# Kernel tuning notes

Measured on AMD Instinct MI355X. Metric: run time of the kernel, lower is better.

Reference implementation:

```python
import jax, jax.numpy as jnp
import numpy as np

DIM, NH, HD = 1536, 12, 128
C = HD // 2            # 64 complex (half) dims per head
BANDS = (C - 2 * (C // 3), C // 3, C // 3)   # (22, 21, 21) for T/H/W
EPS = 1e-6
F, Hg, Wg = 6, 20, 32
S = F * Hg * Wg
MAX_LEN = 1024


def _rope_tables(max_len=MAX_LEN):
    # Wan-style 1D rope params per band, concatenated along channel dim -> [max_len, 64]
    pos = np.arange(max_len, dtype=np.float64)
    cos_l, sin_l = [], []
    for bd in BANDS:
        inv = 1.0 / (10000.0 ** (np.arange(bd, dtype=np.float64) / bd))
        ang = np.outer(pos, inv)
        cos_l.append(np.cos(ang))
        sin_l.append(np.sin(ang))
    return (np.concatenate(cos_l, 1).astype(np.float32),
            np.concatenate(sin_l, 1).astype(np.float32))


def setup_inputs() -> dict:
    key = jax.random.key(0)
    ks = jax.random.split(key, 8)
    std = 0.02
    fc, fs = _rope_tables()
    return {
        "x": jax.random.normal(ks[0], (1, S, DIM), jnp.float32),
        "Wq": jax.random.normal(ks[1], (DIM, DIM), jnp.float32) * std,
        "bq": jnp.zeros((DIM,), jnp.float32),
        "Wk": jax.random.normal(ks[2], (DIM, DIM), jnp.float32) * std,
        "bk": jnp.zeros((DIM,), jnp.float32),
        "Wv": jax.random.normal(ks[3], (DIM, DIM), jnp.float32) * std,
        "bv": jnp.zeros((DIM,), jnp.float32),
        "Wo": jax.random.normal(ks[4], (DIM, DIM), jnp.float32) * std,
        "bo": jnp.zeros((DIM,), jnp.float32),
        "gq": jnp.ones((DIM,), jnp.float32),
        "gk": jnp.ones((DIM,), jnp.float32),
        "freqs_cos": jnp.asarray(fc),
        "freqs_sin": jnp.asarray(fs),
        "f": F, "h": Hg, "w": Wg,
    }


def _rmsnorm(t, g):
    t = t.astype(jnp.float32)
    return t * jax.lax.rsqrt(jnp.mean(t * t, axis=-1, keepdims=True) + EPS) * g


def _grid_freqs(tab, f, h, w):
    # tab: [max_len, 64] -> [f*h*w, 64] via T/H/W band broadcast (mirrors torch expand+cat)
    o1, o2 = BANDS[0], BANDS[0] + BANDS[1]
    t = jnp.broadcast_to(tab[:f, None, None, :o1], (f, h, w, BANDS[0]))
    hh = jnp.broadcast_to(tab[None, :h, None, o1:o2], (f, h, w, BANDS[1]))
    ww = jnp.broadcast_to(tab[None, None, :w, o2:C], (f, h, w, BANDS[2]))
    return jnp.concatenate([t, hh, ww], axis=-1).reshape(f * h * w, 1, C)


def _rope_apply(t, fc, fs):
    # t: [B, S, n, d]; complex mul (a+ib)*(cos+isin) on pairs of channels
    B, Sl, n, d = t.shape
    tr = t.astype(jnp.float32).reshape(B, Sl, n, C, 2)
    a, b = tr[..., 0], tr[..., 1]
    fc = fc[None]  # [1, S, 1, C]
    fs = fs[None]
    out_r = a * fc - b * fs
    out_i = a * fs + b * fc
    return jnp.stack([out_r, out_i], axis=-1).reshape(B, Sl, n, d)


def reference(x, Wq, bq, Wk, bk, Wv, bv, Wo, bo, gq, gk, freqs_cos, freqs_sin, f, h, w):
    B, Sl, _ = x.shape
    q = _rmsnorm(x @ Wq.T + bq, gq).reshape(B, Sl, NH, HD)
    k = _rmsnorm(x @ Wk.T + bk, gk).reshape(B, Sl, NH, HD)
    v = (x @ Wv.T + bv).reshape(B, Sl, NH, HD)

    fc = _grid_freqs(freqs_cos, f, h, w)
    fs = _grid_freqs(freqs_sin, f, h, w)
    q = _rope_apply(q, fc, fs)
    k = _rope_apply(k, fc, fs)

    scale = 1.0 / jnp.sqrt(jnp.float32(HD))
    scores = jnp.einsum('bqnd,bknd->bnqk', q, k) * scale
    p = jax.nn.softmax(scores, axis=-1)
    o = jnp.einsum('bnqk,bknd->bqnd', p, v.astype(jnp.float32))
    o = o.reshape(B, Sl, DIM)
    return o @ Wo.T + bo
```

## Files before the change

kernel.cpp:

```cpp
#include <hip/hip_runtime.h>
#include <hip/hip_bf16.h>
#include <cstdint>

#define DIM 1536
#define NHEADS 12
#define HD 128
#define SEQ 3840
#define SCL2F 0.1275365308119098f
#define THRRAW 90.50966799187809f

typedef float f32x4 __attribute__((ext_vector_type(4)));
typedef __bf16 bf16x8 __attribute__((ext_vector_type(8)));
typedef __bf16 bf16x4 __attribute__((ext_vector_type(4)));
typedef __bf16 bf16x2 __attribute__((ext_vector_type(2)));
typedef unsigned int u32;
typedef u32 u32x4 __attribute__((ext_vector_type(4)));

#define GLLD(g, l) __builtin_amdgcn_global_load_lds( \
    (const __attribute__((address_space(1))) void*)(g), \
    (__attribute__((address_space(3))) void*)(l), 16, 0, 0)

__global__ __launch_bounds__(256) void cvt_bf16_5(
    const float* __restrict__ s0, const float* __restrict__ s1, const float* __restrict__ s2,
    const float* __restrict__ s3, const float* __restrict__ s4,
    __bf16* __restrict__ d0, __bf16* __restrict__ d1, __bf16* __restrict__ d2,
    __bf16* __restrict__ d3, __bf16* __restrict__ d4,
    int n4_0, int n4_w) {
    const float* src; __bf16* dst; int n4;
    switch (blockIdx.y) {
        case 0: src = s0; dst = d0; n4 = n4_0; break;
        case 1: src = s1; dst = d1; n4 = n4_w; break;
        case 2: src = s2; dst = d2; n4 = n4_w; break;
        case 3: src = s3; dst = d3; n4 = n4_w; break;
        default: src = s4; dst = d4; n4 = n4_w; break;
    }
    int i = blockIdx.x * 256 + threadIdx.x;
    if (i < n4) {
        f32x4 v = ((const f32x4*)src)[i];
        bf16x4 o;
        o[0] = (__bf16)v[0]; o[1] = (__bf16)v[1];
        o[2] = (__bf16)v[2]; o[3] = (__bf16)v[3];
        ((bf16x4*)dst)[i] = o;
    }
}

template <int OUTF32>
__global__ __launch_bounds__(256, 2) void gemm256(
    const __bf16* __restrict__ A,
    const __bf16* __restrict__ B0, const __bf16* __restrict__ B1, const __bf16* __restrict__ B2,
    const float* __restrict__ bias0, const float* __restrict__ bias1, const float* __restrict__ bias2,
    void* __restrict__ C0v, void* __restrict__ C1v, void* __restrict__ C2v,
    int N, int K) {
    const __bf16* B = B0; const float* bias = bias0; void* Cv = C0v;
    if (blockIdx.z == 1) { B = B1; bias = bias1; Cv = C1v; }
    else if (blockIdx.z == 2) { B = B2; bias = bias2; Cv = C2v; }

    __shared__ __bf16 sA[3][256 * 32];
    __shared__ __bf16 sB[3][128 * 32];

    const int t = threadIdx.x;
    const int wid = t >> 6, lane = t & 63;
    const int lr = lane & 15, lg = lane >> 4;
    const int wr = (wid >> 1) * 128, wc = (wid & 1) * 64;

    const __bf16* pa = A + ((long long)blockIdx.y * 256 + (t >> 2)) * K + (t & 3) * 8;
    const __bf16* pb = B + ((long long)blockIdx.x * 128 + (t >> 2)) * K + (t & 3) * 8;
    const int ldsbase = wid * 512;

    auto stage = [&](int kk, int bufi) {
#pragma unroll
        for (int r = 0; r < 4; r++)
            GLLD(pa + (long long)(r * 64) * K + kk, &sA[bufi][r * 2048 + ldsbase]);
#pragma unroll
        for (int r = 0; r < 2; r++)
            GLLD(pb + (long long)(r * 64) * K + kk, &sB[bufi][r * 2048 + ldsbase]);
    };

    f32x4 acc[8][4] = {};
    const int NT = K / 32;

    stage(0, 0);
    stage(32, 1);
    asm volatile("s_waitcnt vmcnt(6)" ::: "memory");
    __builtin_amdgcn_s_barrier();
    __builtin_amdgcn_sched_barrier(0);

    int c0 = 0, c2 = 2;
#pragma unroll 1
    for (int i = 0; i < NT; i++) {
        const __bf16* sAc = &sA[0][0] + c0 * (256 * 32);
        const __bf16* sBc = &sB[0][0] + c0 * (128 * 32);
        bf16x8 af[8], bfr[4];
#pragma unroll
        for (int mI = 0; mI < 8; mI++)
            af[mI] = *(const bf16x8*)(sAc + (wr + mI * 16 + lr) * 32 + lg * 8);
#pragma unroll
        for (int nI = 0; nI < 4; nI++)
            bfr[nI] = *(const bf16x8*)(sBc + (wc + nI * 16 + lr) * 32 + lg * 8);
        if (i + 2 < NT) stage((i + 2) * 32, c2);

        __builtin_amdgcn_s_setprio(1);
#pragma unroll
        for (int mI = 0; mI < 8; mI++) {
            acc[mI][0] = __builtin_amdgcn_mfma_f32_16x16x32_bf16(af[mI], bfr[0], acc[mI][0], 0, 0, 0);
            acc[mI][1] = __builtin_amdgcn_mfma_f32_16x16x32_bf16(af[mI], bfr[1], acc[mI][1], 0, 0, 0);
        }
        __builtin_amdgcn_s_setprio(0);
        __builtin_amdgcn_s_barrier();
        __builtin_amdgcn_s_setprio(1);
#pragma unroll
        for (int mI = 0; mI < 8; mI++) {
            acc[mI][2] = __builtin_amdgcn_mfma_f32_16x16x32_bf16(af[mI], bfr[2], acc[mI][2], 0, 0, 0);
            acc[mI][3] = __builtin_amdgcn_mfma_f32_16x16x32_bf16(af[mI], bfr[3], acc[mI][3], 0, 0, 0);
        }
        __builtin_amdgcn_s_setprio(0);

        if (i + 2 < NT) asm volatile("s_waitcnt vmcnt(6)" ::: "memory");
        else            asm volatile("s_waitcnt vmcnt(0)" ::: "memory");
        __builtin_amdgcn_s_barrier();
        __builtin_amdgcn_sched_barrier(0);
        c0 = (c0 == 2) ? 0 : c0 + 1;
        c2 = (c2 == 2) ? 0 : c2 + 1;
    }

    const int cb = blockIdx.x * 128 + wc;
    const int rb_ = blockIdx.y * 256 + wr;
#pragma unroll
    for (int nI = 0; nI < 4; nI++) {
        int col = cb + nI * 16 + lr;
        float bv = bias[col];
#pragma unroll
        for (int mI = 0; mI < 8; mI++) {
            int row0 = rb_ + mI * 16 + lg * 4;
#pragma unroll
            for (int r = 0; r < 4; r++) {
                float v = acc[mI][nI][r] + bv;
                if (OUTF32) ((float*)Cv)[(long long)(row0 + r) * N + col] = v;
                else ((__bf16*)Cv)[(long long)(row0 + r) * N + col] = (__bf16)v;
            }
        }
    }
}

__global__ __launch_bounds__(256) void norm_rope2(
    const __bf16* __restrict__ qpre, const __bf16* __restrict__ kpre,
    const float* __restrict__ gq, const float* __restrict__ gk,
    const float* __restrict__ fcos, const float* __restrict__ fsin,
    __bf16* __restrict__ Qb, __bf16* __restrict__ Kb) {
    const __bf16* pre = blockIdx.y ? kpre : qpre;
    const float* gvec = blockIdx.y ? gk : gq;
    __bf16* out = blockIdx.y ? Kb : Qb;
    const int s = blockIdx.x;
    const int t = threadIdx.x;
    float a[3], b[3];
    float ss = 0.f;
#pragma unroll
    for (int j = 0; j < 3; j++) {
        int p = t + 256 * j;
        bf16x2 v = *(const bf16x2*)(pre + (size_t)s * DIM + 2 * p);
        a[j] = (float)v[0]; b[j] = (float)v[1];
        ss += a[j] * a[j] + b[j] * b[j];
    }
    for (int off = 32; off; off >>= 1) ss += __shfl_down(ss, off);
    __shared__ float red[4];
    if ((t & 63) == 0) red[t >> 6] = ss;
    __syncthreads();
    float mean = (red[0] + red[1] + red[2] + red[3]) * (1.f / DIM);
    float rms = rsqrtf(mean + 1e-6f);
    const int fi = s / 640, hi2 = (s % 640) >> 5, wi = s & 31;
#pragma unroll
    for (int j = 0; j < 3; j++) {
        int p = t + 256 * j;
        int c = p & 63;
        int pos = (c < 22) ? fi : ((c < 43) ? hi2 : wi);
        float fc = fcos[pos * 64 + c];
        float fs = fsin[pos * 64 + c];
        float av = a[j] * rms * gvec[2 * p];
        float bv = b[j] * rms * gvec[2 * p + 1];
        float orr = av * fc - bv * fs;
        float oi = av * fs + bv * fc;
        int hh = p >> 6;
        bf16x2 o; o[0] = (__bf16)orr; o[1] = (__bf16)oi;
        *(bf16x2*)(out + ((size_t)hh * SEQ + s) * HD + 2 * c) = o;
    }
}

__global__ __launch_bounds__(256) void transpose_bf16(
    const __bf16* __restrict__ in, __bf16* __restrict__ out) {
    __shared__ __bf16 tile[64][68];
    const int t = threadIdx.x;
    const int sb = blockIdx.x * 64, cb = blockIdx.y * 64;
    const int tx = t & 15, ty = t >> 4;
#pragma unroll
    for (int i = 0; i < 4; i++) {
        int r = ty + i * 16;
        bf16x4 v = *(const bf16x4*)(in + (size_t)(sb + r) * DIM + cb + tx * 4);
        *(bf16x4*)&tile[r][tx * 4] = v;
    }
    __syncthreads();
    int s0 = sb + tx * 4;
    int j = (s0 >> 2) & 7;
    int u = (j < 4) ? (j << 1) : ((j << 1) - 7);
    int sp = (s0 & ~31) + (u << 2);
#pragma unroll
    for (int i = 0; i < 4; i++) {
        int c = ty + i * 16;
        bf16x4 v;
        v[0] = tile[tx * 4 + 0][c]; v[1] = tile[tx * 4 + 1][c];
        v[2] = tile[tx * 4 + 2][c]; v[3] = tile[tx * 4 + 3][c];
        *(bf16x4*)(out + (size_t)(cb + c) * SEQ + sp) = v;
    }
}

__global__ __launch_bounds__(384, 1) void attn(
    const __bf16* __restrict__ Q, const __bf16* __restrict__ Kk,
    const __bf16* __restrict__ Vp, __bf16* __restrict__ O) {
    __shared__ __bf16 Ks[2][64 * 128];
    __shared__ __bf16 Vs[2][128 * 64];
    const int bid = blockIdx.x;
    const int task = (bid & 7) * 30 + (bid >> 3);
    const int h = task / 20;
    const int qb = task % 20;
    const int t = threadIdx.x;
    const int wv = t >> 6;
    const int lane = t & 63;
    const int lq = lane & 15, g = lane >> 4;
    const int q0 = qb * 192 + wv * 32;
    const __bf16* Qh = Q + (size_t)h * SEQ * HD;
    const __bf16* Kh = Kk + (size_t)h * SEQ * HD;
    const __bf16* Vh = Vp + (size_t)h * HD * SEQ;
    bf16x8 qf[2][4];
#pragma unroll
    for (int qg = 0; qg < 2; qg++)
#pragma unroll
        for (int c = 0; c < 4; c++)
            qf[qg][c] = *(const bf16x8*)(Qh + (size_t)(q0 + qg * 16 + lq) * HD + c * 32 + g * 8);
    f32x4 acc[8][2] = {};
    float m[2] = {-1e30f, -1e30f};
    float lp[2] = {0.f, 0.f};
    const int krow_in = lane >> 4;
    const int vrow_in = lane >> 3;
    const int vce = (((lane & 7) ^ (lane >> 3))) * 8;
    auto stage = [&](int kv0, int b) {
        for (int c = wv; c < 32; c += 6) {
            if (c < 16) {
                int r = c * 4 + krow_in;
                int cb = ((lane & 15) * 16) ^ ((r & 7) << 4);
                GLLD(Kh + (size_t)(kv0 + r) * HD + (cb >> 1), &Ks[b][c * 512]);
            } else {
                int cc = c - 16;
                int rd = cc * 8 + vrow_in;
                GLLD(Vh + (size_t)rd * SEQ + kv0 + vce, &Vs[b][cc * 512]);
            }
        }
    };
    stage(0, 0);
    int buf = 0;
    const int kswz = (lq & 7) << 3;
#pragma unroll 1
    for (int i = 0; i < 60; i++) {
        __syncthreads();
        if (i + 1 < 60) stage((i + 1) * 64, buf ^ 1);
        const __bf16* Kb_ = &Ks[buf][0];
        const __bf16* Vb_ = &Vs[buf][0];
#pragma unroll
        for (int s = 0; s < 2; s++) {
            f32x4 sc[2][2] = {};
            __builtin_amdgcn_s_setprio(1);
#pragma unroll
            for (int c = 0; c < 4; c++) {
                int cb = (c * 32 + g * 8) ^ kswz;
                bf16x8 k0 = *(const bf16x8*)(Kb_ + (s * 32 + lq) * 128 + cb);
                bf16x8 k1 = *(const bf16x8*)(Kb_ + (s * 32 + 16 + lq) * 128 + cb);
                sc[0][0] = __builtin_amdgcn_mfma_f32_16x16x32_bf16(k0, qf[0][c], sc[0][0], 0, 0, 0);
                sc[0][1] = __builtin_amdgcn_mfma_f32_16x16x32_bf16(k0, qf[1][c], sc[0][1], 0, 0, 0);
                sc[1][0] = __builtin_amdgcn_mfma_f32_16x16x32_bf16(k1, qf[0][c], sc[1][0], 0, 0, 0);
                sc[1][1] = __builtin_amdgcn_mfma_f32_16x16x32_bf16(k1, qf[1][c], sc[1][1], 0, 0, 0);
            }
            __builtin_amdgcn_s_setprio(0);

            bf16x8 vf[8];
#pragma unroll
            for (int dt = 0; dt < 8; dt++)
                vf[dt] = *(const bf16x8*)(Vb_ + (dt * 16 + lq) * 64 + ((s * 32 + g * 8) ^ kswz));

            bf16x8 pa[2];
#pragma unroll
            for (int qg = 0; qg < 2; qg++) {
                float pm = fmaxf(fmaxf(fmaxf(sc[0][qg][0], sc[0][qg][1]), fmaxf(sc[0][qg][2], sc[0][qg][3])),
                                 fmaxf(fmaxf(sc[1][qg][0], sc[1][qg][1]), fmaxf(sc[1][qg][2], sc[1][qg][3])));
                if (!__all(pm <= m[qg] + THRRAW)) {
                    pm = fmaxf(pm, __shfl_xor(pm, 16));
                    pm = fmaxf(pm, __shfl_xor(pm, 32));
                    float mn = fmaxf(m[qg], pm);
                    float al = __builtin_amdgcn_exp2f(SCL2F * (m[qg] - mn));
                    m[qg] = mn; lp[qg] *= al;
#pragma unroll
                    for (int dt = 0; dt < 8; dt++)
#pragma unroll
                        for (int r = 0; r < 4; r++) acc[dt][qg][r] *= al;
                }
                float ms = SCL2F * m[qg];
                float p[8], ls = 0.f;
#pragma unroll
                for (int r = 0; r < 4; r++) { p[r] = __builtin_amdgcn_exp2f(SCL2F * sc[0][qg][r] - ms); ls += p[r]; }
#pragma unroll
                for (int r = 0; r < 4; r++) { p[4 + r] = __builtin_amdgcn_exp2f(SCL2F * sc[1][qg][r] - ms); ls += p[4 + r]; }
                lp[qg] += ls;
#pragma unroll
                for (int i2 = 0; i2 < 8; i2++) pa[qg][i2] = (__bf16)p[i2];
            }
            __builtin_amdgcn_s_setprio(1);
#pragma unroll
            for (int dt = 0; dt < 8; dt++) {
                acc[dt][0] = __builtin_amdgcn_mfma_f32_16x16x32_bf16(vf[dt], pa[0], acc[dt][0], 0, 0, 0);
                acc[dt][1] = __builtin_amdgcn_mfma_f32_16x16x32_bf16(vf[dt], pa[1], acc[dt][1], 0, 0, 0);
            }
            __builtin_amdgcn_s_setprio(0);
        }
        buf ^= 1;
    }
#pragma unroll
    for (int qg = 0; qg < 2; qg++) {
        float lps = lp[qg];
        lps += __shfl_xor(lps, 16);
        lps += __shfl_xor(lps, 32);
        float inv = 1.f / lps;
#pragma unroll
        for (int dt = 0; dt < 8; dt++) {
            bf16x4 o;
#pragma unroll
            for (int r = 0; r < 4; r++) o[r] = (__bf16)(acc[dt][qg][r] * inv);
            *(bf16x4*)(O + (size_t)(q0 + qg * 16 + lq) * DIM + h * HD + dt * 16 + g * 4) = o;
        }
    }
}

extern "C" void kernel_launch(void* const* d_in, const int* in_sizes, int n_in,
                              void* d_out, int out_size, void* d_ws, size_t ws_size,
                              hipStream_t stream) {
    const float* x = (const float*)d_in[0];
    const float* Wq = (const float*)d_in[1];
    const float* bq = (const float*)d_in[2];
    const float* Wk = (const float*)d_in[3];
    const float* bk = (const float*)d_in[4];
    const float* Wv = (const float*)d_in[5];
    const float* bv = (const float*)d_in[6];
    const float* Wo = (const float*)d_in[7];
    const float* bo = (const float*)d_in[8];
    const float* gq = (const float*)d_in[9];
    const float* gk = (const float*)d_in[10];
    const float* fcos = (const float*)d_in[11];
    const float* fsin = (const float*)d_in[12];
    float* out = (float*)d_out;

    char* p = (char*)d_ws;
    const size_t SZ_SD = (size_t)SEQ * DIM * 2;
    const size_t SZ_W = (size_t)DIM * DIM * 2;
    __bf16* xb   = (__bf16*)p;  p += SZ_SD;
    __bf16* Wqb  = (__bf16*)p;  p += SZ_W;
    __bf16* Wkb  = (__bf16*)p;  p += SZ_W;
    __bf16* Wvb  = (__bf16*)p;  p += SZ_W;
    __bf16* Wob  = (__bf16*)p;  p += SZ_W;
    __bf16* qpre = (__bf16*)p;  p += SZ_SD;
    __bf16* kpre = (__bf16*)p;  p += SZ_SD;
    __bf16* vpre = (__bf16*)p;  p += SZ_SD;
    __bf16* Kb   = (__bf16*)p;  p += SZ_SD;
    __bf16* Vtb  = (__bf16*)p;  p += SZ_SD;
    __bf16* Qb = xb;
    __bf16* ob = qpre;

    const int n4_x = SEQ * DIM / 4;
    const int n4_w = DIM * DIM / 4;
    cvt_bf16_5<<<dim3((n4_x + 255) / 256, 5), 256, 0, stream>>>(
        x, Wq, Wk, Wv, Wo, xb, Wqb, Wkb, Wvb, Wob, n4_x, n4_w);

    gemm256<0><<<dim3(DIM / 128, SEQ / 256, 3), 256, 0, stream>>>(
        xb, Wqb, Wkb, Wvb, bq, bk, bv, qpre, kpre, vpre, DIM, DIM);

    norm_rope2<<<dim3(SEQ, 2), 256, 0, stream>>>(qpre, kpre, gq, gk, fcos, fsin, Qb, Kb);
    transpose_bf16<<<dim3(SEQ / 64, DIM / 64), 256, 0, stream>>>(vpre, Vtb);

    attn<<<dim3(240), 384, 0, stream>>>(Qb, Kb, Vtb, ob);

    gemm256<1><<<dim3(DIM / 128, SEQ / 256, 1), 256, 0, stream>>>(
        ob, Wob, Wob, Wob, bo, bo, bo, out, out, out, DIM, DIM);
}
```

Before: 287.1 us.

## Split attention into smaller 64-query blocks with 32-key tiles for higher occupancy

The attention kernel moves from 240 blocks of 6 waves, each wave covering 32 queries over 64-key tiles, to 720 blocks of 4 waves, each wave covering 16 queries over 32-key tiles, with launch bounds allowing 4 blocks per CU. The aim is to fill all CUs more evenly and put more waves on each CU so that latency and the serial softmax section are better hidden. In exchange, each K/V tile held in LDS is reused by fewer queries, K/V are fetched from global memory three times as often, there are twice as many barrier iterations, and the new V LDS layout drops the XOR swizzle, which may cause bank conflicts.

After: 284.9 us. Within noise of the previous version (-0.8%).

```diff
diff --git a/kernel.cpp b/kernel.cpp
--- a/kernel.cpp
+++ b/kernel.cpp
@@ -212,127 +212,120 @@
     }
 }
 
-__global__ __launch_bounds__(384, 1) void attn(
+__global__ __launch_bounds__(256, 4) void attn(
     const __bf16* __restrict__ Q, const __bf16* __restrict__ Kk,
     const __bf16* __restrict__ Vp, __bf16* __restrict__ O) {
-    __shared__ __bf16 Ks[2][64 * 128];
-    __shared__ __bf16 Vs[2][128 * 64];
+    __shared__ __bf16 Ks[2][32 * 128];
+    __shared__ __bf16 Vs[2][128 * 32];
     const int bid = blockIdx.x;
-    const int task = (bid & 7) * 30 + (bid >> 3);
-    const int h = task / 20;
-    const int qb = task % 20;
+    const int task = (bid & 7) * 90 + (bid >> 3);
+    const int h = task / 60;
+    const int qb = task % 60;
     const int t = threadIdx.x;
     const int wv = t >> 6;
     const int lane = t & 63;
     const int lq = lane & 15, g = lane >> 4;
-    const int q0 = qb * 192 + wv * 32;
+    const int q0 = qb * 64 + wv * 16;
     const __bf16* Qh = Q + (size_t)h * SEQ * HD;
     const __bf16* Kh = Kk + (size_t)h * SEQ * HD;
     const __bf16* Vh = Vp + (size_t)h * HD * SEQ;
-    bf16x8 qf[2][4];
-#pragma unroll
-    for (int qg = 0; qg < 2; qg++)
-#pragma unroll
-        for (int c = 0; c < 4; c++)
-            qf[qg][c] = *(const bf16x8*)(Qh + (size_t)(q0 + qg * 16 + lq) * HD + c * 32 + g * 8);
-    f32x4 acc[8][2] = {};
-    float m[2] = {-1e30f, -1e30f};
-    float lp[2] = {0.f, 0.f};
+
+    bf16x8 qf[4];
+#pragma unroll
+    for (int c = 0; c < 4; c++)
+        qf[c] = *(const bf16x8*)(Qh + (size_t)(q0 + lq) * HD + c * 32 + g * 8);
+
+    f32x4 acc[8] = {};
+    float m = -1e30f;
+    float lp = 0.f;
+
     const int krow_in = lane >> 4;
-    const int vrow_in = lane >> 3;
-    const int vce = (((lane & 7) ^ (lane >> 3))) * 8;
+    const int vrow_in = lane >> 2;
+    const int vce = (lane & 3) * 8;
     auto stage = [&](int kv0, int b) {
-        for (int c = wv; c < 32; c += 6) {
-            if (c < 16) {
+#pragma unroll
+        for (int c = wv; c < 16; c += 4) {
+            if (c < 8) {
                 int r = c * 4 + krow_in;
                 int cb = ((lane & 15) * 16) ^ ((r & 7) << 4);
                 GLLD(Kh + (size_t)(kv0 + r) * HD + (cb >> 1), &Ks[b][c * 512]);
             } else {
-                int cc = c - 16;
-                int rd = cc * 8 + vrow_in;
+                int cc = c - 8;
+                int rd = cc * 16 + vrow_in;
                 GLLD(Vh + (size_t)rd * SEQ + kv0 + vce, &Vs[b][cc * 512]);
             }
         }
     };
+
     stage(0, 0);
     int buf = 0;
     const int kswz = (lq & 7) << 3;
 #pragma unroll 1
-    for (int i = 0; i < 60; i++) {
+    for (int i = 0; i < 120; i++) {
         __syncthreads();
-        if (i + 1 < 60) stage((i + 1) * 64, buf ^ 1);
+        if (i + 1 < 120) stage((i + 1) * 32, buf ^ 1);
         const __bf16* Kb_ = &Ks[buf][0];
         const __bf16* Vb_ = &Vs[buf][0];
-#pragma unroll
-        for (int s = 0; s < 2; s++) {
-            f32x4 sc[2][2] = {};
-            __builtin_amdgcn_s_setprio(1);
-#pragma unroll
-            for (int c = 0; c < 4; c++) {
-                int cb = (c * 32 + g * 8) ^ kswz;
-                bf16x8 k0 = *(const bf16x8*)(Kb_ + (s * 32 + lq) * 128 + cb);
-                bf16x8 k1 = *(const bf16x8*)(Kb_ + (s * 32 + 16 + lq) * 128 + cb);
-                sc[0][0] = __builtin_amdgcn_mfma_f32_16x16x32_bf16(k0, qf[0][c], sc[0][0], 0, 0, 0);
-                sc[0][1] = __builtin_amdgcn_mfma_f32_16x16x32_bf16(k0, qf[1][c], sc[0][1], 0, 0, 0);
-                sc[1][0] = __builtin_amdgcn_mfma_f32_16x16x32_bf16(k1, qf[0][c], sc[1][0], 0, 0, 0);
-                sc[1][1] = __builtin_amdgcn_mfma_f32_16x16x32_bf16(k1, qf[1][c], sc[1][1], 0, 0, 0);
-            }
-            __builtin_amdgcn_s_setprio(0);
-
-            bf16x8 vf[8];
+
+        f32x4 sc0 = {0.f, 0.f, 0.f, 0.f}, sc1 = {0.f, 0.f, 0.f, 0.f};
+        __builtin_amdgcn_s_setprio(1);
+#pragma unroll
+        for (int c = 0; c < 4; c++) {
+            int cb = (c * 32 + g * 8) ^ kswz;
+            bf16x8 k0 = *(const bf16x8*)(Kb_ + lq * 128 + cb);
+            bf16x8 k1 = *(const bf16x8*)(Kb_ + (16 + lq) * 128 + cb);
+            sc0 = __builtin_amdgcn_mfma_f32_16x16x32_bf16(k0, qf[c], sc0, 0, 0, 0);
+            sc1 = __builtin_amdgcn_mfma_f32_16x16x32_bf16(k1, qf[c], sc1, 0, 0, 0);
+        }
+        __builtin_amdgcn_s_setprio(0);
+
+        bf16x8 vf[8];
+#pragma unroll
+        for (int dt = 0; dt < 8; dt++)
+            vf[dt] = *(const bf16x8*)(Vb_ + (dt * 16 + lq) * 32 + g * 8);
+
+        float pm = fmaxf(fmaxf(fmaxf(sc0[0], sc0[1]), fmaxf(sc0[2], sc0[3])),
+                         fmaxf(fmaxf(sc1[0], sc1[1]), fmaxf(sc1[2], sc1[3])));
+        if (!__all(pm <= m + THRRAW)) {
+            pm = fmaxf(pm, __shfl_xor(pm, 16));
+            pm = fmaxf(pm, __shfl_xor(pm, 32));
+            float mn = fmaxf(m, pm);
+            float al = __builtin_amdgcn_exp2f(SCL2F * (m - mn));
+            m = mn; lp *= al;
 #pragma unroll
             for (int dt = 0; dt < 8; dt++)
-                vf[dt] = *(const bf16x8*)(Vb_ + (dt * 16 + lq) * 64 + ((s * 32 + g * 8) ^ kswz));
-
-            bf16x8 pa[2];
-#pragma unroll
-            for (int qg = 0; qg < 2; qg++) {
-                float pm = fmaxf(fmaxf(fmaxf(sc[0][qg][0], sc[0][qg][1]), fmaxf(sc[0][qg][2], sc[0][qg][3])),
-                                 fmaxf(fmaxf(sc[1][qg][0], sc[1][qg][1]), fmaxf(sc[1][qg][2], sc[1][qg][3])));
-                if (!__all(pm <= m[qg] + THRRAW)) {
-                    pm = fmaxf(pm, __shfl_xor(pm, 16));
-                    pm = fmaxf(pm, __shfl_xor(pm, 32));
-                    float mn = fmaxf(m[qg], pm);
-                    float al = __builtin_amdgcn_exp2f(SCL2F * (m[qg] - mn));
-                    m[qg] = mn; lp[qg] *= al;
-#pragma unroll
-                    for (int dt = 0; dt < 8; dt++)
-#pragma unroll
-                        for (int r = 0; r < 4; r++) acc[dt][qg][r] *= al;
-                }
-                float ms = SCL2F * m[qg];
-                float p[8], ls = 0.f;
-#pragma unroll
-                for (int r = 0; r < 4; r++) { p[r] = __builtin_amdgcn_exp2f(SCL2F * sc[0][qg][r] - ms); ls += p[r]; }
-#pragma unroll
-                for (int r = 0; r < 4; r++) { p[4 + r] = __builtin_amdgcn_exp2f(SCL2F * sc[1][qg][r] - ms); ls += p[4 + r]; }
-                lp[qg] += ls;
-#pragma unroll
-                for (int i2 = 0; i2 < 8; i2++) pa[qg][i2] = (__bf16)p[i2];
-            }
-            __builtin_amdgcn_s_setprio(1);
-#pragma unroll
-            for (int dt = 0; dt < 8; dt++) {
-                acc[dt][0] = __builtin_amdgcn_mfma_f32_16x16x32_bf16(vf[dt], pa[0], acc[dt][0], 0, 0, 0);
-                acc[dt][1] = __builtin_amdgcn_mfma_f32_16x16x32_bf16(vf[dt], pa[1], acc[dt][1], 0, 0, 0);
-            }
-            __builtin_amdgcn_s_setprio(0);
-        }
+#pragma unroll
+                for (int r = 0; r < 4; r++) acc[dt][r] *= al;
+        }
+        float ms = SCL2F * m;
+        float p[8], ls = 0.f;
+#pragma unroll
+        for (int r = 0; r < 4; r++) { p[r] = __builtin_amdgcn_exp2f(SCL2F * sc0[r] - ms); ls += p[r]; }
+#pragma unroll
+        for (int r = 0; r < 4; r++) { p[4 + r] = __builtin_amdgcn_exp2f(SCL2F * sc1[r] - ms); ls += p[4 + r]; }
+        lp += ls;
+        bf16x8 pa;
+#pragma unroll
+        for (int i2 = 0; i2 < 8; i2++) pa[i2] = (__bf16)p[i2];
+
+        __builtin_amdgcn_s_setprio(1);
+#pragma unroll
+        for (int dt = 0; dt < 8; dt++)
+            acc[dt] = __builtin_amdgcn_mfma_f32_16x16x32_bf16(vf[dt], pa, acc[dt], 0, 0, 0);
+        __builtin_amdgcn_s_setprio(0);
         buf ^= 1;
     }
-#pragma unroll
-    for (int qg = 0; qg < 2; qg++) {
-        float lps = lp[qg];
-        lps += __shfl_xor(lps, 16);
-        lps += __shfl_xor(lps, 32);
-        float inv = 1.f / lps;
-#pragma unroll
-        for (int dt = 0; dt < 8; dt++) {
-            bf16x4 o;
-#pragma unroll
-            for (int r = 0; r < 4; r++) o[r] = (__bf16)(acc[dt][qg][r] * inv);
-            *(bf16x4*)(O + (size_t)(q0 + qg * 16 + lq) * DIM + h * HD + dt * 16 + g * 4) = o;
-        }
+
+    float lps = lp;
+    lps += __shfl_xor(lps, 16);
+    lps += __shfl_xor(lps, 32);
+    float inv = 1.f / lps;
+#pragma unroll
+    for (int dt = 0; dt < 8; dt++) {
+        bf16x4 o;
+#pragma unroll
+        for (int r = 0; r < 4; r++) o[r] = (__bf16)(acc[dt][r] * inv);
+        *(bf16x4*)(O + (size_t)(q0 + lq) * DIM + h * HD + dt * 16 + g * 4) = o;
     }
 }
 
@@ -381,7 +374,7 @@
     norm_rope2<<<dim3(SEQ, 2), 256, 0, stream>>>(qpre, kpre, gq, gk, fcos, fsin, Qb, Kb);
     transpose_bf16<<<dim3(SEQ / 64, DIM / 64), 256, 0, stream>>>(vpre, Vtb);
 
-    attn<<<dim3(240), 384, 0, stream>>>(Qb, Kb, Vtb, ob);
+    attn<<<dim3(720), 256, 0, stream>>>(Qb, Kb, Vtb, ob);
 
     gemm256<1><<<dim3(DIM / 128, SEQ / 256, 1), 256, 0, stream>>>(
         ob, Wob, Wob, Wob, bo, bo, bo, out, out, out, DIM, DIM);
```
